# Performance work log

Hardware: AMD Instinct MI355X
Metric: run time of the kernel (lower is better)

The kernel has to match this reference:

```python
import jax, jax.numpy as jnp
import numpy as np

BN_EPS = 1e-3  # Keras BatchNormalization default epsilon


def _conv_block(x, k):
    """Per-task conv (stride 2, pad 1) -> ReLU -> BatchNorm (center/scale=False, training).

    x: [B, E, H, W, Cin]  (B tasks, E examples per task)
    k: [B, kh, kw, Cin, Cout]  per-task kernel
    """
    def conv_one(xe, kt):  # xe: [E,H,W,Cin], kt: [kh,kw,Cin,Cout]
        return jax.lax.conv_general_dilated(
            xe, kt, window_strides=(2, 2), padding=[(1, 1), (1, 1)],
            dimension_numbers=('NHWC', 'HWIO', 'NHWC'))
    y = jax.nn.relu(jax.vmap(conv_one)(x, k))  # [B,E,H',W',Cout]
    # BatchNorm in training mode: moments over all axes except channels
    m = jnp.mean(y, axis=(0, 1, 2, 3))
    v = jnp.var(y, axis=(0, 1, 2, 3))
    return (y - m) * jax.lax.rsqrt(v + BN_EPS)


def setup_inputs() -> dict:
    key = jax.random.key(0)
    ks = jax.random.split(key, 6)
    B, E, H, C, O = 64, 64, 28, 64, 20
    return {
        'x': jax.random.normal(ks[0], (B, E, H, H, 1), dtype=jnp.float32),
        'k1': jax.random.normal(ks[1], (B, 3, 3, 1, C), dtype=jnp.float32) * 0.1,
        'k2': jax.random.normal(ks[2], (B, 3, 3, C, C), dtype=jnp.float32) * 0.05,
        'k3': jax.random.normal(ks[3], (B, 3, 3, C, C), dtype=jnp.float32) * 0.05,
        'k4': jax.random.normal(ks[4], (B, 3, 3, C, C), dtype=jnp.float32) * 0.05,
        'w_ro': jax.random.normal(ks[5], (B, C, O), dtype=jnp.float32) * 0.1,
    }


def reference(x, k1, k2, k3, k4, w_ro):
    h = _conv_block(x, k1)   # [B,E,14,14,C]
    h = _conv_block(h, k2)   # [B,E,7,7,C]
    h = _conv_block(h, k3)   # [B,E,4,4,C]
    h = _conv_block(h, k4)   # [B,E,2,2,C]
    # MaxPooling2D with pool size == full spatial extent -> global spatial max
    feat = jnp.max(h, axis=(2, 3))  # [B,E,C]
    # per-task readout matmul: [B,E,H] x [B,H,O] -> [B,E,O]
    return jnp.einsum('beh,bho->beo', feat, w_ro)
```

## Files before the change

kernel.cpp:

```cpp
#include <hip/hip_runtime.h>

#define BN_EPS 1e-3f

typedef __attribute__((ext_vector_type(8))) short bf16x8;
typedef __attribute__((ext_vector_type(16))) float floatx16;
typedef unsigned short u16;

__device__ __forceinline__ u16 f2bf(float f) {
  unsigned u = __float_as_uint(f);
  u += 0x7fffu + ((u >> 16) & 1u);
  return (u16)(u >> 16);
}
__device__ __forceinline__ float bf2f(u16 h) {
  return __uint_as_float(((unsigned)h) << 16);
}

static constexpr int NSHARD = 64;

__global__ __launch_bounds__(256, 4) void conv1_k(
    const float* __restrict__ x, const float* __restrict__ k1,
    u16* __restrict__ y1, float* __restrict__ statsSh)
{
  __shared__ __align__(16) u16 Ah[256 * 24];
  __shared__ __align__(16) u16 Al[256 * 24];
  __shared__ __align__(16) u16 Wh[64 * 24];
  __shared__ __align__(16) u16 Wl[64 * 24];
  __shared__ __align__(16) float xp[30 * 36];
  __shared__ float redsum[64], redss[64];

  const int be = blockIdx.x, b = be >> 6, tid = threadIdx.x;

  {
    const uint4 z = uint4{0, 0, 0, 0};
    for (int i = tid; i < 768; i += 256) ((uint4*)Ah)[i] = z;
    for (int i = tid; i < 768; i += 256) ((uint4*)Al)[i] = z;
    if (tid < 192) ((uint4*)Wh)[tid] = z;
    if (tid < 192) ((uint4*)Wl)[tid] = z;
    for (int i = tid; i < 270; i += 256) ((uint4*)xp)[i] = z;
    if (tid < 64) { redsum[tid] = 0.f; redss[tid] = 0.f; }
  }
  __syncthreads();

  for (int i = tid; i < 784; i += 256) {
    const int r = i / 28, c = i - 28 * r;
    xp[(r + 1) * 36 + (c + 1)] = x[(size_t)be * 784 + i];
  }
  for (int idx = tid; idx < 576; idx += 256) {
    const int t = idx >> 6, c = idx & 63;
    const float v = k1[(size_t)b * 576 + idx];
    const u16 hi = f2bf(v);
    const u16 lo = f2bf(v - bf2f(hi));
    Wh[c * 24 + t] = hi;
    Wl[c * 24 + t] = lo;
  }
  __syncthreads();

  if (tid < 196) {
    const int oy = tid / 14, ox = tid - 14 * oy;
    const float* base = &xp[(2 * oy) * 36 + 2 * ox];
#pragma unroll
    for (int ky = 0; ky < 3; ++ky)
#pragma unroll
      for (int kx = 0; kx < 3; ++kx) {
        const float v = base[ky * 36 + kx];
        const u16 hi = f2bf(v);
        const u16 lo = f2bf(v - bf2f(hi));
        Ah[tid * 24 + ky * 3 + kx] = hi;
        Al[tid * 24 + ky * 3 + kx] = lo;
      }
  }
  __syncthreads();

  const int wave = tid >> 6, lane = tid & 63;
  const int l31 = lane & 31, kq = (lane >> 5) * 8;

  bf16x8 ah[2], al[2], bh[2], bl[2];
#pragma unroll
  for (int mt = 0; mt < 2; ++mt) {
    const int row = (wave * 2 + mt) * 32 + l31;
    ah[mt] = *(const bf16x8*)&Ah[row * 24 + kq];
    al[mt] = *(const bf16x8*)&Al[row * 24 + kq];
  }
#pragma unroll
  for (int nt = 0; nt < 2; ++nt) {
    const int colB = nt * 32 + l31;
    bh[nt] = *(const bf16x8*)&Wh[colB * 24 + kq];
    bl[nt] = *(const bf16x8*)&Wl[colB * 24 + kq];
  }

  floatx16 acc[2][2];
#pragma unroll
  for (int mt = 0; mt < 2; ++mt)
#pragma unroll
    for (int nt = 0; nt < 2; ++nt) {
#pragma unroll
      for (int r = 0; r < 16; ++r) acc[mt][nt][r] = 0.f;
      acc[mt][nt] = __builtin_amdgcn_mfma_f32_32x32x16_bf16(
          al[mt], bh[nt], acc[mt][nt], 0, 0, 0);
      acc[mt][nt] = __builtin_amdgcn_mfma_f32_32x32x16_bf16(
          ah[mt], bl[nt], acc[mt][nt], 0, 0, 0);
      acc[mt][nt] = __builtin_amdgcn_mfma_f32_32x32x16_bf16(
          ah[mt], bh[nt], acc[mt][nt], 0, 0, 0);
    }

#pragma unroll
  for (int nt = 0; nt < 2; ++nt) {
    const int col = nt * 32 + l31;
    float ls = 0.f, lss = 0.f;
#pragma unroll
    for (int mt = 0; mt < 2; ++mt) {
      const int rb = (wave * 2 + mt) * 32 + 4 * (lane >> 5);
#pragma unroll
      for (int r = 0; r < 16; ++r) {
        const int rw = rb + (r & 3) + 8 * (r >> 2);
        if (rw < 196) {
          const float v = fmaxf(acc[mt][nt][r], 0.f);
          y1[((size_t)be * 196 + rw) * 64 + col] = f2bf(v);
          ls += v;
          lss = fmaf(v, v, lss);
        }
      }
    }
    atomicAdd(&redsum[col], ls);
    atomicAdd(&redss[col], lss);
  }
  __syncthreads();
  if (tid < 64) {
    const int sh = be & (NSHARD - 1);
    atomicAdd(&statsSh[sh * 128 + tid], redsum[tid]);
    atomicAdd(&statsSh[sh * 128 + 64 + tid], redss[tid]);
  }
}

__global__ __launch_bounds__(256) void foldw_k(
    const float* __restrict__ W, const float* __restrict__ statsSh, float invN,
    u16* __restrict__ Wf, float* __restrict__ biasCls)
{
  __shared__ float T[64 * 68];
  __shared__ float P[256];
  __shared__ float s1[64], t1[64];
  __shared__ float tbS[64];

  const int b = blockIdx.x / 3, sg = blockIdx.x % 3;
  const int tid = threadIdx.x;

  {
    const int g = tid >> 7, cidx = tid & 127;
    float acc = 0.f;
    for (int k = 0; k < NSHARD / 2; ++k)
      acc += statsSh[(g * (NSHARD / 2) + k) * 128 + cidx];
    P[tid] = acc;
  }
  __syncthreads();
  if (tid < 64) {
    const float m = (P[tid] + P[tid + 128]) * invN;
    const float var = fmaf(-m, m, (P[64 + tid] + P[192 + tid]) * invN);
    const float s = rsqrtf(var + BN_EPS);
    s1[tid] = s;
    t1[tid] = -m * s;
  }
  __syncthreads();

  const int cin = tid >> 2, q0 = (tid & 3) * 16;
  const int cout = tid >> 2, ci0 = (tid & 3) * 16;
  for (int s = sg * 3; s < sg * 3 + 3; ++s) {
    if (tid < 64) tbS[tid] = 0.f;
    const float* ss = W + ((size_t)b * 9 + s) * 4096;
#pragma unroll
    for (int q = 0; q < 16; q += 4) {
      const float4 v = *(const float4*)(ss + cin * 64 + q0 + q);
      T[(q0 + q + 0) * 68 + cin] = v.x;
      T[(q0 + q + 1) * 68 + cin] = v.y;
      T[(q0 + q + 2) * 68 + cin] = v.z;
      T[(q0 + q + 3) * 68 + cin] = v.w;
    }
    __syncthreads();
    alignas(16) u16 tmp[16];
    float tb = 0.f;
#pragma unroll
    for (int j = 0; j < 16; ++j) {
      const float wv = T[cout * 68 + ci0 + j];
      tmp[j] = f2bf(wv * s1[ci0 + j]);
      tb = fmaf(t1[ci0 + j], wv, tb);
    }
    u16* dst = Wf + ((size_t)b * 9 + s) * 4096 + cout * 64 + ci0;
    *(uint4*)dst       = *(uint4*)&tmp[0];
    *(uint4*)(dst + 8) = *(uint4*)&tmp[8];
    atomicAdd(&tbS[cout], tb);
    __syncthreads();
    if (tid < 64) {
      const int ky = s / 3, kx = s % 3;
      const float tv = tbS[tid];
#pragma unroll
      for (int cls = 0; cls < 9; ++cls) {
        const int ry = cls / 3, rx = cls % 3;
        const bool valid = !((ry == 1 && ky == 0) || (ry == 2 && ky == 2) ||
                             (rx == 1 && kx == 0) || (rx == 2 && kx == 2));
        if (valid) atomicAdd(&biasCls[(size_t)b * 576 + cls * 64 + tid], tv);
      }
    }
    __syncthreads();
  }
}

template <int Hin, int Hout, int G>
__device__ __forceinline__ void conv_core(
    const u16* __restrict__ yin, const u16* __restrict__ Wf,
    const float* __restrict__ biasCls, u16* __restrict__ yout,
    float* __restrict__ statsSh, int blk)
{
  constexpr int PPI  = Hout * Hout;
  constexpr int ROWS = G * PPI;
  constexpr int BPT  = 64 / G;
  constexpr int MR   = G * Hin * Hin;
  constexpr int ZR   = MR;

  __shared__ __align__(16) u16 mapS[(MR + 1) * 72];
  __shared__ __align__(16) u16 Bb[2][64 * 72];
  __shared__ float biasS[576];
  __shared__ float redsum[64], redss[64];

  const int b = blk / BPT, e0 = (blk % BPT) * G;
  const int tid = threadIdx.x, lane = tid & 63, wave = tid >> 6;

  for (int i = tid; i < 576; i += 256) biasS[i] = biasCls[(size_t)b * 576 + i];
  if (tid < 64) { redsum[tid] = 0.f; redss[tid] = 0.f; }
  if (tid < 8) *(uint4*)&mapS[ZR * 72 + tid * 8] = uint4{0, 0, 0, 0};

  {
    const u16* src = yin + (size_t)(b * 64 + e0) * (Hin * Hin) * 64;
    for (int ch = tid; ch < MR * 8; ch += 256) {
      const int r = ch >> 3, c8 = ch & 7;
      *(uint4*)&mapS[r * 72 + c8 * 8] = *(const uint4*)(src + ch * 8);
    }
  }

  const int bco = tid >> 2, bci = (tid & 3) * 16;
  const u16* wb = Wf + (size_t)b * 9 * 4096 + bco * 64 + bci;
  {
    uint4 b0 = *(const uint4*)wb;
    uint4 b1 = *(const uint4*)(wb + 8);
    *(uint4*)&Bb[0][bco * 72 + bci]     = b0;
    *(uint4*)&Bb[0][bco * 72 + bci + 8] = b1;
  }

  const int m0 = (wave & 1) * 32, n0 = (wave >> 1) * 32;
  const int l31 = lane & 31, kq = (lane >> 5) * 8;
  const int lrow = m0 + l31;
  const bool rv = lrow < ROWS;
  const int img = rv ? lrow / PPI : 0;
  const int pp  = rv ? lrow % PPI : 0;
  const int oy = pp / Hout, ox = pp % Hout;

  floatx16 acc;
#pragma unroll
  for (int r = 0; r < 16; ++r) acc[r] = 0.f;

  __syncthreads();

#pragma unroll
  for (int s = 0; s < 9; ++s) {
    uint4 nb0, nb1;
    if (s < 8) {
      const u16* wsl = wb + (s + 1) * 4096;
      nb0 = *(const uint4*)wsl;
      nb1 = *(const uint4*)(wsl + 8);
    }
    const int ky = s / 3, kx = s % 3;
    int pix = ZR;
    if (rv) {
      const int iy = 2 * oy - 1 + ky, ix = 2 * ox - 1 + kx;
      if ((unsigned)iy < (unsigned)Hin && (unsigned)ix < (unsigned)Hin)
        pix = img * (Hin * Hin) + iy * Hin + ix;
    }
    const u16* ap = &mapS[pix * 72 + kq];
    const u16* bp = &Bb[s & 1][(n0 + l31) * 72 + kq];
#pragma unroll
    for (int kk = 0; kk < 4; ++kk) {
      bf16x8 a  = *(const bf16x8*)(ap + kk * 16);
      bf16x8 bv = *(const bf16x8*)(bp + kk * 16);
      acc = __builtin_amdgcn_mfma_f32_32x32x16_bf16(a, bv, acc, 0, 0, 0);
    }
    if (s < 8) {
      u16* d = &Bb[(s + 1) & 1][bco * 72 + bci];
      *(uint4*)d       = nb0;
      *(uint4*)(d + 8) = nb1;
    }
    __syncthreads();
  }

  const int col = n0 + l31;
  const int rb = m0 + 4 * (lane >> 5);
  float ls = 0.f, lss = 0.f;
#pragma unroll
  for (int r = 0; r < 16; ++r) {
    const int rw = rb + (r & 3) + 8 * (r >> 2);
    if (rw < ROWS) {
      const int re = rw / PPI, pr = rw % PPI;
      const int ooy = pr / Hout, oox = pr % Hout;
      const int ry = (ooy == 0) ? 1 : ((2 * ooy + 1 >= Hin) ? 2 : 0);
      const int rx = (oox == 0) ? 1 : ((2 * oox + 1 >= Hin) ? 2 : 0);
      const float v = fmaxf(acc[r] + biasS[(ry * 3 + rx) * 64 + col], 0.f);
      yout[((size_t)(b * 64 + e0 + re) * PPI + pr) * 64 + col] = f2bf(v);
      ls += v;
      lss = fmaf(v, v, lss);
    }
  }
  atomicAdd(&redsum[col], ls);
  atomicAdd(&redss[col], lss);
  __syncthreads();
  if (tid < 64) {
    const int sh = blk & (NSHARD - 1);
    atomicAdd(&statsSh[sh * 128 + tid], redsum[tid]);
    atomicAdd(&statsSh[sh * 128 + 64 + tid], redss[tid]);
  }
}

__global__ __launch_bounds__(256) void cg2_k(
    const u16* __restrict__ yin, const u16* __restrict__ Wf,
    const float* __restrict__ biasCls, u16* __restrict__ yout,
    float* __restrict__ statsSh) {
  conv_core<14, 7, 1>(yin, Wf, biasCls, yout, statsSh, blockIdx.x);
}
__global__ __launch_bounds__(256) void cg3_k(
    const u16* __restrict__ yin, const u16* __restrict__ Wf,
    const float* __restrict__ biasCls, u16* __restrict__ yout,
    float* __restrict__ statsSh) {
  conv_core<7, 4, 4>(yin, Wf, biasCls, yout, statsSh, blockIdx.x);
}
__global__ __launch_bounds__(256) void cg4_k(
    const u16* __restrict__ yin, const u16* __restrict__ Wf,
    const float* __restrict__ biasCls, u16* __restrict__ yout,
    float* __restrict__ statsSh) {
  conv_core<4, 2, 16>(yin, Wf, biasCls, yout, statsSh, blockIdx.x);
}

__global__ __launch_bounds__(256) void readout_k(
    const u16* __restrict__ y4, const float* __restrict__ w_ro,
    const float* __restrict__ statsSh, float invN, float* __restrict__ outp)
{
  __shared__ float wl[64 * 20];
  __shared__ float feat[64 * 64];
  __shared__ float P[256];
  __shared__ float sArr[64], tArr[64];

  const int b = blockIdx.x, tid = threadIdx.x;

  {
    const int g = tid >> 7, cidx = tid & 127;
    float acc = 0.f;
    for (int k = 0; k < NSHARD / 2; ++k)
      acc += statsSh[(g * (NSHARD / 2) + k) * 128 + cidx];
    P[tid] = acc;
  }
  for (int i = tid; i < 1280; i += 256) wl[i] = w_ro[(size_t)b * 1280 + i];
  __syncthreads();
  if (tid < 64) {
    const float m = (P[tid] + P[tid + 128]) * invN;
    const float var = fmaf(-m, m, (P[64 + tid] + P[192 + tid]) * invN);
    const float s = rsqrtf(var + BN_EPS);
    sArr[tid] = s;
    tArr[tid] = -m * s;
  }
  __syncthreads();

  {
    const int e = tid & 63;
    for (int c = tid >> 6; c < 64; c += 4) {
      const u16* p4 = y4 + ((size_t)(b * 64 + e) * 4) * 64 + c;
      const float v = fmaxf(fmaxf(bf2f(p4[0]), bf2f(p4[64])),
                            fmaxf(bf2f(p4[128]), bf2f(p4[192])));
      feat[c * 64 + e] = fmaf(v, sArr[c], tArr[c]);
    }
  }
  __syncthreads();

  const int e = tid >> 2, og = (tid & 3) * 5;
  float acc[5] = {0.f, 0.f, 0.f, 0.f, 0.f};
  for (int c = 0; c < 64; ++c) {
    const float f = feat[c * 64 + e];
#pragma unroll
    for (int j = 0; j < 5; ++j) acc[j] = fmaf(f, wl[c * 20 + og + j], acc[j]);
  }
#pragma unroll
  for (int j = 0; j < 5; ++j)
    outp[((size_t)b * 64 + e) * 20 + og + j] = acc[j];
}

extern "C" void kernel_launch(void* const* d_in, const int* in_sizes, int n_in,
                              void* d_out, int out_size, void* d_ws, size_t ws_size,
                              hipStream_t stream) {
  (void)in_sizes; (void)n_in; (void)out_size; (void)ws_size;
  const float* x   = (const float*)d_in[0];
  const float* k1  = (const float*)d_in[1];
  const float* k2  = (const float*)d_in[2];
  const float* k3  = (const float*)d_in[3];
  const float* k4  = (const float*)d_in[4];
  const float* wro = (const float*)d_in[5];
  float* out = (float*)d_out;
  char* ws = (char*)d_ws;

  float* stats = (float*)ws;
  float* bias2 = (float*)(ws + 131072);
  float* bias3 = bias2 + 36864;
  float* bias4 = bias3 + 36864;
  u16* k2f = (u16*)(ws + 131072 + 442368);
  u16* k3f = k2f + (size_t)2359296;
  u16* k4f = k3f + (size_t)2359296;
  u16* y2 = k4f + (size_t)2359296;
  u16* y1 = y2 + (size_t)12845056;
  u16* y3 = y1;
  u16* y4 = y3 + (size_t)4194304;

  float* st1 = stats;
  float* st2 = stats + 8192;
  float* st3 = stats + 16384;
  float* st4 = stats + 24576;

  hipMemsetAsync(stats, 0, 131072 + 442368, stream);

  conv1_k<<<4096, 256, 0, stream>>>(x, k1, y1, st1);
  foldw_k<<<192, 256, 0, stream>>>(k2, st1, 1.f / 802816.f, k2f, bias2);
  cg2_k<<<4096, 256, 0, stream>>>(y1, k2f, bias2, y2, st2);
  foldw_k<<<192, 256, 0, stream>>>(k3, st2, 1.f / 200704.f, k3f, bias3);
  cg3_k<<<1024, 256, 0, stream>>>(y2, k3f, bias3, y3, st3);
  foldw_k<<<192, 256, 0, stream>>>(k4, st3, 1.f / 65536.f, k4f, bias4);
  cg4_k<<<256, 256, 0, stream>>>(y3, k4f, bias4, y4, st4);
  readout_k<<<64, 256, 0, stream>>>(y4, wro, st4, 1.f / 16384.f, out);
}
```

Measured before the change: 254.3 us.

## Stage conv1 output in LDS, load conv weights to registers, swizzle activation LDS

conv1 now writes its bf16 output tile into reused shared memory and then copies it out with coalesced 16-byte stores, replacing scattered 2-byte global stores. In conv_core, the double-buffered LDS weight staging and the per-tap __syncthreads are removed. Each lane instead loads its B fragments straight from global memory into a two-deep register prefetch. The activation map drops its padding in favour of an XOR swizzle to avoid bank conflicts. The conv kernels also gain an occupancy hint of 4 blocks per CU, which adds register pressure and leaves global weight-load latency exposed inside the MFMA loop.

```diff
diff --git a/kernel.cpp b/kernel.cpp
--- a/kernel.cpp
+++ b/kernel.cpp
@@ -15,27 +15,28 @@
   return __uint_as_float(((unsigned)h) << 16);
 }
 
+__device__ __forceinline__ int swzh(int r) { return ((r >> 1) + (r >> 3)) & 7; }
+
 static constexpr int NSHARD = 64;
 
 __global__ __launch_bounds__(256, 4) void conv1_k(
     const float* __restrict__ x, const float* __restrict__ k1,
     u16* __restrict__ y1, float* __restrict__ statsSh)
 {
-  __shared__ __align__(16) u16 Ah[256 * 24];
-  __shared__ __align__(16) u16 Al[256 * 24];
-  __shared__ __align__(16) u16 Wh[64 * 24];
-  __shared__ __align__(16) u16 Wl[64 * 24];
+  __shared__ __align__(16) u16 smem1[15360];
   __shared__ __align__(16) float xp[30 * 36];
   __shared__ float redsum[64], redss[64];
 
+  u16* Ah = smem1;
+  u16* Al = smem1 + 6144;
+  u16* Wh = smem1 + 12288;
+  u16* Wl = smem1 + 13824;
+
   const int be = blockIdx.x, b = be >> 6, tid = threadIdx.x;
 
   {
     const uint4 z = uint4{0, 0, 0, 0};
-    for (int i = tid; i < 768; i += 256) ((uint4*)Ah)[i] = z;
-    for (int i = tid; i < 768; i += 256) ((uint4*)Al)[i] = z;
-    if (tid < 192) ((uint4*)Wh)[tid] = z;
-    if (tid < 192) ((uint4*)Wl)[tid] = z;
+    for (int i = tid; i < 1920; i += 256) ((uint4*)smem1)[i] = z;
     for (int i = tid; i < 270; i += 256) ((uint4*)xp)[i] = z;
     if (tid < 64) { redsum[tid] = 0.f; redss[tid] = 0.f; }
   }
@@ -103,6 +104,9 @@
           ah[mt], bh[nt], acc[mt][nt], 0, 0, 0);
     }
 
+  __syncthreads();
+  u16* yS = smem1;
+
 #pragma unroll
   for (int nt = 0; nt < 2; ++nt) {
     const int col = nt * 32 + l31;
@@ -115,7 +119,7 @@
         const int rw = rb + (r & 3) + 8 * (r >> 2);
         if (rw < 196) {
           const float v = fmaxf(acc[mt][nt][r], 0.f);
-          y1[((size_t)be * 196 + rw) * 64 + col] = f2bf(v);
+          yS[rw * 64 + col] = f2bf(v);
           ls += v;
           lss = fmaf(v, v, lss);
         }
@@ -125,6 +129,12 @@
     atomicAdd(&redss[col], lss);
   }
   __syncthreads();
+
+  {
+    uint4* dst = (uint4*)(y1 + (size_t)be * 12544);
+    const uint4* s4 = (const uint4*)yS;
+    for (int i = tid; i < 1568; i += 256) dst[i] = s4[i];
+  }
   if (tid < 64) {
     const int sh = be & (NSHARD - 1);
     atomicAdd(&statsSh[sh * 128 + tid], redsum[tid]);
@@ -215,8 +225,7 @@
   constexpr int MR   = G * Hin * Hin;
   constexpr int ZR   = MR;
 
-  __shared__ __align__(16) u16 mapS[(MR + 1) * 72];
-  __shared__ __align__(16) u16 Bb[2][64 * 72];
+  __shared__ __align__(16) u16 mapS[(MR + 1) * 64];
   __shared__ float biasS[576];
   __shared__ float redsum[64], redss[64];
 
@@ -225,33 +234,34 @@
 
   for (int i = tid; i < 576; i += 256) biasS[i] = biasCls[(size_t)b * 576 + i];
   if (tid < 64) { redsum[tid] = 0.f; redss[tid] = 0.f; }
-  if (tid < 8) *(uint4*)&mapS[ZR * 72 + tid * 8] = uint4{0, 0, 0, 0};
+  if (tid < 8) *(uint4*)&mapS[(ZR << 6) + (tid << 3)] = uint4{0, 0, 0, 0};
 
   {
     const u16* src = yin + (size_t)(b * 64 + e0) * (Hin * Hin) * 64;
     for (int ch = tid; ch < MR * 8; ch += 256) {
       const int r = ch >> 3, c8 = ch & 7;
-      *(uint4*)&mapS[r * 72 + c8 * 8] = *(const uint4*)(src + ch * 8);
-    }
-  }
-
-  const int bco = tid >> 2, bci = (tid & 3) * 16;
-  const u16* wb = Wf + (size_t)b * 9 * 4096 + bco * 64 + bci;
-  {
-    uint4 b0 = *(const uint4*)wb;
-    uint4 b1 = *(const uint4*)(wb + 8);
-    *(uint4*)&Bb[0][bco * 72 + bci]     = b0;
-    *(uint4*)&Bb[0][bco * 72 + bci + 8] = b1;
+      const int sc = c8 ^ swzh(r);
+      *(uint4*)&mapS[(r << 6) + (sc << 3)] = *(const uint4*)(src + ch * 8);
+    }
   }
 
   const int m0 = (wave & 1) * 32, n0 = (wave >> 1) * 32;
-  const int l31 = lane & 31, kq = (lane >> 5) * 8;
+  const int l31 = lane & 31, kh = lane >> 5;
   const int lrow = m0 + l31;
   const bool rv = lrow < ROWS;
   const int img = rv ? lrow / PPI : 0;
   const int pp  = rv ? lrow % PPI : 0;
   const int oy = pp / Hout, ox = pp % Hout;
 
+  const u16* wbase = Wf + (size_t)b * 9 * 4096 + (n0 + l31) * 64 + kh * 8;
+
+  bf16x8 bq[2][4];
+#pragma unroll
+  for (int ps = 0; ps < 2; ++ps)
+#pragma unroll
+    for (int kk = 0; kk < 4; ++kk)
+      bq[ps][kk] = *(const bf16x8*)(wbase + ps * 4096 + kk * 16);
+
   floatx16 acc;
 #pragma unroll
   for (int r = 0; r < 16; ++r) acc[r] = 0.f;
@@ -260,12 +270,6 @@
 
 #pragma unroll
   for (int s = 0; s < 9; ++s) {
-    uint4 nb0, nb1;
-    if (s < 8) {
-      const u16* wsl = wb + (s + 1) * 4096;
-      nb0 = *(const uint4*)wsl;
-      nb1 = *(const uint4*)(wsl + 8);
-    }
     const int ky = s / 3, kx = s % 3;
     int pix = ZR;
     if (rv) {
@@ -273,20 +277,21 @@
       if ((unsigned)iy < (unsigned)Hin && (unsigned)ix < (unsigned)Hin)
         pix = img * (Hin * Hin) + iy * Hin + ix;
     }
-    const u16* ap = &mapS[pix * 72 + kq];
-    const u16* bp = &Bb[s & 1][(n0 + l31) * 72 + kq];
-#pragma unroll
-    for (int kk = 0; kk < 4; ++kk) {
-      bf16x8 a  = *(const bf16x8*)(ap + kk * 16);
-      bf16x8 bv = *(const bf16x8*)(bp + kk * 16);
-      acc = __builtin_amdgcn_mfma_f32_32x32x16_bf16(a, bv, acc, 0, 0, 0);
-    }
-    if (s < 8) {
-      u16* d = &Bb[(s + 1) & 1][bco * 72 + bci];
-      *(uint4*)d       = nb0;
-      *(uint4*)(d + 8) = nb1;
-    }
-    __syncthreads();
+    const int hh = swzh(pix);
+    const int abase = pix << 6;
+    bf16x8 a[4];
+#pragma unroll
+    for (int kk = 0; kk < 4; ++kk)
+      a[kk] = *(const bf16x8*)&mapS[abase + (((kh + 2 * kk) ^ hh) << 3)];
+#pragma unroll
+    for (int kk = 0; kk < 4; ++kk)
+      acc = __builtin_amdgcn_mfma_f32_32x32x16_bf16(a[kk], bq[s & 1][kk],
+                                                    acc, 0, 0, 0);
+    if (s < 7) {
+#pragma unroll
+      for (int kk = 0; kk < 4; ++kk)
+        bq[s & 1][kk] = *(const bf16x8*)(wbase + (s + 2) * 4096 + kk * 16);
+    }
   }
 
   const int col = n0 + l31;
@@ -316,19 +321,19 @@
   }
 }
 
-__global__ __launch_bounds__(256) void cg2_k(
+__global__ __launch_bounds__(256, 4) void cg2_k(
     const u16* __restrict__ yin, const u16* __restrict__ Wf,
     const float* __restrict__ biasCls, u16* __restrict__ yout,
     float* __restrict__ statsSh) {
   conv_core<14, 7, 1>(yin, Wf, biasCls, yout, statsSh, blockIdx.x);
 }
-__global__ __launch_bounds__(256) void cg3_k(
+__global__ __launch_bounds__(256, 4) void cg3_k(
     const u16* __restrict__ yin, const u16* __restrict__ Wf,
     const float* __restrict__ biasCls, u16* __restrict__ yout,
     float* __restrict__ statsSh) {
   conv_core<7, 4, 4>(yin, Wf, biasCls, yout, statsSh, blockIdx.x);
 }
-__global__ __launch_bounds__(256) void cg4_k(
+__global__ __launch_bounds__(256, 4) void cg4_k(
     const u16* __restrict__ yin, const u16* __restrict__ Wf,
     const float* __restrict__ biasCls, u16* __restrict__ yout,
     float* __restrict__ statsSh) {
```

Measured after the change: 286.1 us. +12.5%, slower.

## Recompute conv1 inside conv2 kernel instead of storing y1 activations

Applied to the files above, without the earlier changes.

Conv1 becomes a stats-only pass that no longer writes its bf16 output to global memory. The conv2 kernel recomputes conv1 from x and k1 with split-bf16 MFMAs straight into shared memory, then runs the conv2 GEMM on it. This removes the write and re-read of the large y1 intermediate at the cost of running conv1 twice. Conv1 is recomputed from fp32 x rather than read back as bf16, which changes rounding slightly.

```diff
diff --git a/kernel.cpp b/kernel.cpp
--- a/kernel.cpp
+++ b/kernel.cpp
@@ -17,25 +17,24 @@
 
 static constexpr int NSHARD = 64;
 
-__global__ __launch_bounds__(256, 4) void conv1_k(
+__global__ __launch_bounds__(256, 4) void conv1s_k(
     const float* __restrict__ x, const float* __restrict__ k1,
-    u16* __restrict__ y1, float* __restrict__ statsSh)
+    float* __restrict__ statsSh)
 {
-  __shared__ __align__(16) u16 Ah[256 * 24];
-  __shared__ __align__(16) u16 Al[256 * 24];
-  __shared__ __align__(16) u16 Wh[64 * 24];
-  __shared__ __align__(16) u16 Wl[64 * 24];
+  __shared__ __align__(16) u16 smem1[15360];
   __shared__ __align__(16) float xp[30 * 36];
   __shared__ float redsum[64], redss[64];
 
+  u16* Ah = smem1;
+  u16* Al = smem1 + 6144;
+  u16* Wh = smem1 + 12288;
+  u16* Wl = smem1 + 13824;
+
   const int be = blockIdx.x, b = be >> 6, tid = threadIdx.x;
 
   {
     const uint4 z = uint4{0, 0, 0, 0};
-    for (int i = tid; i < 768; i += 256) ((uint4*)Ah)[i] = z;
-    for (int i = tid; i < 768; i += 256) ((uint4*)Al)[i] = z;
-    if (tid < 192) ((uint4*)Wh)[tid] = z;
-    if (tid < 192) ((uint4*)Wl)[tid] = z;
+    for (int i = tid; i < 1920; i += 256) ((uint4*)smem1)[i] = z;
     for (int i = tid; i < 270; i += 256) ((uint4*)xp)[i] = z;
     if (tid < 64) { redsum[tid] = 0.f; redss[tid] = 0.f; }
   }
@@ -115,7 +114,6 @@
         const int rw = rb + (r & 3) + 8 * (r >> 2);
         if (rw < 196) {
           const float v = fmaxf(acc[mt][nt][r], 0.f);
-          y1[((size_t)be * 196 + rw) * 64 + col] = f2bf(v);
           ls += v;
           lss = fmaf(v, v, lss);
         }
@@ -200,6 +198,199 @@
       }
     }
     __syncthreads();
+  }
+}
+
+__global__ __launch_bounds__(256, 3) void cg2f_k(
+    const float* __restrict__ x, const float* __restrict__ k1,
+    const u16* __restrict__ Wf, const float* __restrict__ biasCls,
+    u16* __restrict__ yout, float* __restrict__ statsSh)
+{
+  constexpr int Hin = 14, Hout = 7, PPI = 49, ROWS = 49;
+  constexpr int MR = 196, ZR = 196;
+
+  __shared__ __align__(16) float xp[30 * 32];
+  __shared__ __align__(16) u16 mapS[(MR + 1) * 72];
+  __shared__ __align__(16) u16 Bb[2][64 * 72];
+  __shared__ float biasS[576];
+  __shared__ float redsum[64], redss[64];
+
+  const int be = blockIdx.x, b = be >> 6, tid = threadIdx.x;
+  const int lane = tid & 63, wave = tid >> 6;
+  const int l31 = lane & 31, kh = lane >> 5;
+
+  {
+    const uint4 z = uint4{0, 0, 0, 0};
+    for (int i = tid; i < 240; i += 256) ((uint4*)xp)[i] = z;
+    if (tid < 8) *(uint4*)&mapS[ZR * 72 + tid * 8] = z;
+    if (tid < 64) { redsum[tid] = 0.f; redss[tid] = 0.f; }
+  }
+  for (int i = tid; i < 576; i += 256) biasS[i] = biasCls[(size_t)b * 576 + i];
+
+  const int bco = tid >> 2, bci = (tid & 3) * 16;
+  const u16* wb = Wf + (size_t)b * 9 * 4096 + bco * 64 + bci;
+  {
+    uint4 b0 = *(const uint4*)wb;
+    uint4 b1 = *(const uint4*)(wb + 8);
+    *(uint4*)&Bb[0][bco * 72 + bci]     = b0;
+    *(uint4*)&Bb[0][bco * 72 + bci + 8] = b1;
+  }
+  __syncthreads();
+
+  for (int i = tid; i < 784; i += 256) {
+    const int r = i / 28, c = i - 28 * r;
+    xp[(r + 1) * 32 + (c + 1)] = x[(size_t)be * 784 + i];
+  }
+  __syncthreads();
+
+  bf16x8 c1ah[2], c1al[2], c1bh[2], c1bl[2];
+#pragma unroll
+  for (int mt = 0; mt < 2; ++mt) {
+    const int row = (wave * 2 + mt) * 32 + l31;
+    const int p = row < 196 ? row : 195;
+    const int poy = p / 14, pox = p - 14 * poy;
+    const float* xb = &xp[(2 * poy) * 32 + 2 * pox];
+    bf16x8 h, lo;
+#pragma unroll
+    for (int j = 0; j < 8; ++j) { h[j] = 0; lo[j] = 0; }
+    if (kh == 0) {
+#pragma unroll
+      for (int t = 0; t < 8; ++t) {
+        const float v = xb[(t / 3) * 32 + (t % 3)];
+        const u16 hi = f2bf(v);
+        h[t] = (short)hi;
+        lo[t] = (short)f2bf(v - bf2f(hi));
+      }
+    } else {
+      const float v = xb[2 * 32 + 2];
+      const u16 hi = f2bf(v);
+      h[0] = (short)hi;
+      lo[0] = (short)f2bf(v - bf2f(hi));
+    }
+    c1ah[mt] = h;
+    c1al[mt] = lo;
+  }
+#pragma unroll
+  for (int nt = 0; nt < 2; ++nt) {
+    const int colB = nt * 32 + l31;
+    const float* kg = k1 + (size_t)b * 576 + colB;
+    bf16x8 h, lo;
+#pragma unroll
+    for (int j = 0; j < 8; ++j) { h[j] = 0; lo[j] = 0; }
+    if (kh == 0) {
+#pragma unroll
+      for (int t = 0; t < 8; ++t) {
+        const float v = kg[t * 64];
+        const u16 hi = f2bf(v);
+        h[t] = (short)hi;
+        lo[t] = (short)f2bf(v - bf2f(hi));
+      }
+    } else {
+      const float v = kg[8 * 64];
+      const u16 hi = f2bf(v);
+      h[0] = (short)hi;
+      lo[0] = (short)f2bf(v - bf2f(hi));
+    }
+    c1bh[nt] = h;
+    c1bl[nt] = lo;
+  }
+
+  floatx16 c1acc[2][2];
+#pragma unroll
+  for (int mt = 0; mt < 2; ++mt)
+#pragma unroll
+    for (int nt = 0; nt < 2; ++nt) {
+#pragma unroll
+      for (int r = 0; r < 16; ++r) c1acc[mt][nt][r] = 0.f;
+      c1acc[mt][nt] = __builtin_amdgcn_mfma_f32_32x32x16_bf16(
+          c1al[mt], c1bh[nt], c1acc[mt][nt], 0, 0, 0);
+      c1acc[mt][nt] = __builtin_amdgcn_mfma_f32_32x32x16_bf16(
+          c1ah[mt], c1bl[nt], c1acc[mt][nt], 0, 0, 0);
+      c1acc[mt][nt] = __builtin_amdgcn_mfma_f32_32x32x16_bf16(
+          c1ah[mt], c1bh[nt], c1acc[mt][nt], 0, 0, 0);
+    }
+
+#pragma unroll
+  for (int nt = 0; nt < 2; ++nt) {
+    const int col = nt * 32 + l31;
+#pragma unroll
+    for (int mt = 0; mt < 2; ++mt) {
+      const int rb = (wave * 2 + mt) * 32 + 4 * (lane >> 5);
+#pragma unroll
+      for (int r = 0; r < 16; ++r) {
+        const int rw = rb + (r & 3) + 8 * (r >> 2);
+        if (rw < 196)
+          mapS[rw * 72 + col] = f2bf(fmaxf(c1acc[mt][nt][r], 0.f));
+      }
+    }
+  }
+
+  const int m0 = (wave & 1) * 32, n0 = (wave >> 1) * 32;
+  const int kq = kh * 8;
+  const int lrow = m0 + l31;
+  const bool rv = lrow < ROWS;
+  const int oy = rv ? lrow / Hout : 0, ox = rv ? lrow % Hout : 0;
+
+  floatx16 acc;
+#pragma unroll
+  for (int r = 0; r < 16; ++r) acc[r] = 0.f;
+
+  __syncthreads();
+
+#pragma unroll
+  for (int s = 0; s < 9; ++s) {
+    uint4 nb0, nb1;
+    if (s < 8) {
+      const u16* wsl = wb + (s + 1) * 4096;
+      nb0 = *(const uint4*)wsl;
+      nb1 = *(const uint4*)(wsl + 8);
+    }
+    const int ky = s / 3, kx = s % 3;
+    int pix = ZR;
+    if (rv) {
+      const int iy = 2 * oy - 1 + ky, ix = 2 * ox - 1 + kx;
+      if ((unsigned)iy < (unsigned)Hin && (unsigned)ix < (unsigned)Hin)
+        pix = iy * Hin + ix;
+    }
+    const u16* ap = &mapS[pix * 72 + kq];
+    const u16* bp = &Bb[s & 1][(n0 + l31) * 72 + kq];
+#pragma unroll
+    for (int kk = 0; kk < 4; ++kk) {
+      bf16x8 a  = *(const bf16x8*)(ap + kk * 16);
+      bf16x8 bv = *(const bf16x8*)(bp + kk * 16);
+      acc = __builtin_amdgcn_mfma_f32_32x32x16_bf16(a, bv, acc, 0, 0, 0);
+    }
+    if (s < 8) {
+      u16* d = &Bb[(s + 1) & 1][bco * 72 + bci];
+      *(uint4*)d       = nb0;
+      *(uint4*)(d + 8) = nb1;
+    }
+    __syncthreads();
+  }
+
+  const int col = n0 + l31;
+  const int rb = m0 + 4 * (lane >> 5);
+  float ls = 0.f, lss = 0.f;
+#pragma unroll
+  for (int r = 0; r < 16; ++r) {
+    const int rw = rb + (r & 3) + 8 * (r >> 2);
+    if (rw < ROWS) {
+      const int ooy = rw / Hout, oox = rw % Hout;
+      const int ry = (ooy == 0) ? 1 : ((2 * ooy + 1 >= Hin) ? 2 : 0);
+      const int rx = (oox == 0) ? 1 : ((2 * oox + 1 >= Hin) ? 2 : 0);
+      const float v = fmaxf(acc[r] + biasS[(ry * 3 + rx) * 64 + col], 0.f);
+      yout[((size_t)be * PPI + rw) * 64 + col] = f2bf(v);
+      ls += v;
+      lss = fmaf(v, v, lss);
+    }
+  }
+  atomicAdd(&redsum[col], ls);
+  atomicAdd(&redss[col], lss);
+  __syncthreads();
+  if (tid < 64) {
+    const int sh = be & (NSHARD - 1);
+    atomicAdd(&statsSh[sh * 128 + tid], redsum[tid]);
+    atomicAdd(&statsSh[sh * 128 + 64 + tid], redss[tid]);
   }
 }
 
@@ -316,12 +507,6 @@
   }
 }
 
-__global__ __launch_bounds__(256) void cg2_k(
-    const u16* __restrict__ yin, const u16* __restrict__ Wf,
-    const float* __restrict__ biasCls, u16* __restrict__ yout,
-    float* __restrict__ statsSh) {
-  conv_core<14, 7, 1>(yin, Wf, biasCls, yout, statsSh, blockIdx.x);
-}
 __global__ __launch_bounds__(256) void cg3_k(
     const u16* __restrict__ yin, const u16* __restrict__ Wf,
     const float* __restrict__ biasCls, u16* __restrict__ yout,
@@ -408,8 +593,7 @@
   u16* k3f = k2f + (size_t)2359296;
   u16* k4f = k3f + (size_t)2359296;
   u16* y2 = k4f + (size_t)2359296;
-  u16* y1 = y2 + (size_t)12845056;
-  u16* y3 = y1;
+  u16* y3 = y2 + (size_t)12845056;
   u16* y4 = y3 + (size_t)4194304;
 
   float* st1 = stats;
@@ -419,9 +603,9 @@
 
   hipMemsetAsync(stats, 0, 131072 + 442368, stream);
 
-  conv1_k<<<4096, 256, 0, stream>>>(x, k1, y1, st1);
+  conv1s_k<<<4096, 256, 0, stream>>>(x, k1, st1);
   foldw_k<<<192, 256, 0, stream>>>(k2, st1, 1.f / 802816.f, k2f, bias2);
-  cg2_k<<<4096, 256, 0, stream>>>(y1, k2f, bias2, y2, st2);
+  cg2f_k<<<4096, 256, 0, stream>>>(x, k1, k2f, bias2, y2, st2);
   foldw_k<<<192, 256, 0, stream>>>(k3, st2, 1.f / 200704.f, k3f, bias3);
   cg3_k<<<1024, 256, 0, stream>>>(y2, k3f, bias3, y3, st3);
   foldw_k<<<192, 256, 0, stream>>>(k4, st3, 1.f / 65536.f, k4f, bias4);
```

Result: no change. 257.5 us (+1.3%).
